# Kernel optimization log

Measured on AMD Instinct MI355X. Metric: run time of the kernel, lower is better.

Reference implementation:

```python
import jax, jax.numpy as jnp
import numpy as np
from jax import lax

STORAGE = 8
HIDDEN_HEAD = 32
N_BLOCKS = 16


def _conv(x, w, b, padding):
    # x: NCHW, w: OIHW
    y = lax.conv_general_dilated(
        x, w, window_strides=(1, 1), padding=padding,
        dimension_numbers=("NCHW", "OIHW", "NCHW"))
    return y + b[None, :, None, None]


def _min_pool3(x):
    # 3x3 sliding-window min, stride 1, same padding (pad value +inf so it
    return lax.reduce_window(x, float("inf"), lax.min,
                             (1, 1, 3, 3), (1, 1, 1, 1), "SAME")


def setup_inputs() -> dict:
    key = jax.random.key(0)
    ks = jax.random.split(key, 7)
    B, H, W = 8, 512, 512
    x = jax.random.normal(ks[0], (B, 1, H, W), dtype=jnp.float32)
    # initial 1x1 conv: 1 -> 8
    w0 = jax.random.normal(ks[1], (STORAGE, 1, 1, 1), dtype=jnp.float32) * 1.0
    b0 = jax.random.normal(ks[2], (STORAGE,), dtype=jnp.float32) * 0.1
    # head conv 3x3: 8 -> 32
    w1 = jax.random.normal(ks[3], (HIDDEN_HEAD, STORAGE, 3, 3), dtype=jnp.float32) * (1.0 / np.sqrt(STORAGE * 9))
    b1 = jax.random.normal(ks[4], (HIDDEN_HEAD,), dtype=jnp.float32) * 0.1
    # head conv 1x1: 32 -> 1
    w2 = jax.random.normal(ks[5], (1, HIDDEN_HEAD, 1, 1), dtype=jnp.float32) * (1.0 / np.sqrt(HIDDEN_HEAD))
    b2 = jax.random.normal(ks[6], (1,), dtype=jnp.float32) * 0.1
    return {"x": x, "w0": w0, "b0": b0, "w1": w1, "b1": b1, "w2": w2, "b2": b2}


def reference(x, w0, b0, w1, b1, w2, b2):
    h = _conv(x, w0, b0, "SAME")  # [B,8,H,W]
    for _ in range(N_BLOCKS):
        h = h + _min_pool3(h)
    h = _conv(h, w1, b1, "SAME")  # [B,32,H,W]
    h = jax.nn.relu(h)
    return _conv(h, w2, b2, "SAME")  # [B,1,H,W]
```

## Files before the change

### kernel.cpp

```cpp
#include <hip/hip_runtime.h>
#include <math.h>


#define N_PIX (512*512)
#define INF __builtin_inff()

typedef __attribute__((ext_vector_type(2))) float f2;

__device__ __forceinline__ float dpp_shr1(float v, float fill) {
    return __int_as_float(__builtin_amdgcn_update_dpp(
        __float_as_int(fill), __float_as_int(v), 0x138, 0xF, 0xF, false));
}
__device__ __forceinline__ float dpp_shl1(float v, float fill) {
    return __int_as_float(__builtin_amdgcn_update_dpp(
        __float_as_int(fill), __float_as_int(v), 0x130, 0xF, 0xF, false));
}

struct Row8 { float4 a, b; };

__device__ __forceinline__ Row8 row_update8(const Row8 up, const Row8 mid, const Row8 dn)
{
    float4 va, vb;
    va.x = fminf(fminf(up.a.x, mid.a.x), dn.a.x);
    va.y = fminf(fminf(up.a.y, mid.a.y), dn.a.y);
    va.z = fminf(fminf(up.a.z, mid.a.z), dn.a.z);
    va.w = fminf(fminf(up.a.w, mid.a.w), dn.a.w);
    vb.x = fminf(fminf(up.b.x, mid.b.x), dn.b.x);
    vb.y = fminf(fminf(up.b.y, mid.b.y), dn.b.y);
    vb.z = fminf(fminf(up.b.z, mid.b.z), dn.b.z);
    vb.w = fminf(fminf(up.b.w, mid.b.w), dn.b.w);
    float vmL = dpp_shr1(vb.w, INF);
    float vmR = dpp_shl1(va.x, INF);
    float tm1 = fminf(vmL, va.x);
    float t0 = fminf(va.x, va.y), t1 = fminf(va.y, va.z);
    float t2 = fminf(va.z, va.w), t3 = fminf(va.w, vb.x);
    float t4 = fminf(vb.x, vb.y), t5 = fminf(vb.y, vb.z);
    float t6 = fminf(vb.z, vb.w), t7 = fminf(vb.w, vmR);
    Row8 o;
    o.a.x = mid.a.x + fminf(tm1, t0);
    o.a.y = mid.a.y + fminf(t0, t1);
    o.a.z = mid.a.z + fminf(t1, t2);
    o.a.w = mid.a.w + fminf(t2, t3);
    o.b.x = mid.b.x + fminf(t3, t4);
    o.b.y = mid.b.y + fminf(t4, t5);
    o.b.z = mid.b.z + fminf(t5, t6);
    o.b.w = mid.b.w + fminf(t6, t7);
    return o;
}

__device__ __forceinline__ void halo_write(f2* hp, const Row8& v) {
    hp[0*64] = (f2){v.a.x, v.a.y};
    hp[1*64] = (f2){v.a.z, v.a.w};
    hp[2*64] = (f2){v.b.x, v.b.y};
    hp[3*64] = (f2){v.b.z, v.b.w};
}
__device__ __forceinline__ Row8 halo_read(const f2* hp) {
    f2 p0 = hp[0*64], p1 = hp[1*64], p2 = hp[2*64], p3 = hp[3*64];
    Row8 v;
    v.a = make_float4(p0.x, p0.y, p1.x, p1.y);
    v.b = make_float4(p2.x, p2.y, p3.x, p3.y);
    return v;
}

__global__ __launch_bounds__(256, 1) void erode16_kernel(
    const float* __restrict__ x, float* __restrict__ A,
    const float* __restrict__ w0, const float* __restrict__ b0,
    const float* __restrict__ w1, const float* __restrict__ b1,
    float* __restrict__ W)
{
    if (blockIdx.x == 0 && blockIdx.y == 0) {
        for (int t = threadIdx.x; t < 288; t += 256) {
            int oc = t / 9, k = t - oc*9;
            float wp = 0.f, wq = 0.f;
            for (int ic = 0; ic < 8; ++ic) {
                float a = w0[ic];
                float w = w1[oc*72 + ic*9 + k];
                if (a > 0.f) wp += w * a;
                else         wq += w * (-a);
            }
            W[(oc*9 + k)*2 + 0] = wp;
            W[(oc*9 + k)*2 + 1] = wq;
            if (k == 0) {
                float beta[9];
                for (int kk = 0; kk < 9; ++kk) {
                    float s = 0.f;
                    for (int ic = 0; ic < 8; ++ic) s += b0[ic] * w1[oc*72 + ic*9 + kk];
                    beta[kk] = 65536.0f * s;
                }
                for (int r = 0; r < 3; ++r) {
                    W[576 + oc*4 + r] = beta[r*3] + beta[r*3+1] + beta[r*3+2]
                                      + ((r == 1) ? b1[oc] : 0.f);
                    W[704 + oc*4 + r] = beta[r*3 + 0];
                    W[832 + oc*4 + r] = beta[r*3 + 2];
                }
            }
        }
    }

    __shared__ f2 halo[2][4][2][4][64];
    const int tid   = threadIdx.x;
    const int lane  = tid & 63;
    const int w     = tid >> 6;
    const int ty    = blockIdx.x;
    const int plane = blockIdx.y;
    const int colg  = lane * 8;
    const int row0g = ty*32 - 16 + w*16;

    const float* sp = x + (plane & 7)*N_PIX;
    const float sgn = (plane >= 8) ? -1.f : 1.f;

    Row8 h[16];
    #pragma unroll
    for (int r = 0; r < 16; ++r) {
        int gy = row0g + r;
        if ((unsigned)gy < 512u) {
            const float* rp = sp + gy*512 + colg;
            float4 a = *(const float4*)rp;
            float4 b = *(const float4*)(rp + 4);
            h[r].a = make_float4(a.x*sgn, a.y*sgn, a.z*sgn, a.w*sgn);
            h[r].b = make_float4(b.x*sgn, b.y*sgn, b.z*sgn, b.w*sgn);
        } else {
            h[r].a = make_float4(INF, INF, INF, INF);
            h[r].b = h[r].a;
        }
    }

    const Row8 inf8 = { make_float4(INF,INF,INF,INF), make_float4(INF,INF,INF,INF) };
    for (int s = 0; s < 16; ++s) {
        int par = s & 1;
        halo_write(&halo[par][w][0][0][lane], h[0]);
        halo_write(&halo[par][w][1][0][lane], h[15]);
        Row8 o1 = h[1];
        Row8 prev = h[0];
        #pragma unroll
        for (int r = 1; r <= 14; ++r) {
            Row8 tmp = h[r];
            h[r] = row_update8(prev, h[r], h[r+1]);
            prev = tmp;
        }
        __syncthreads();
        Row8 up = inf8, dn = inf8;
        if (w > 0) up = halo_read(&halo[par][w-1][1][0][lane]);
        if (w < 3) dn = halo_read(&halo[par][w+1][0][0][lane]);
        h[0]  = row_update8(up,   h[0],  o1);
        h[15] = row_update8(prev, h[15], dn);
    }

    if (w == 1 || w == 2) {
        float* dp = A + plane*N_PIX;
        #pragma unroll
        for (int r = 0; r < 16; ++r) {
            float* op = dp + (row0g + r)*512 + colg;
            *(float4*)op       = h[r].a;
            *(float4*)(op + 4) = h[r].b;
        }
    }
}

__global__ __launch_bounds__(256) void head_kernel(
    const float* __restrict__ A, const float* __restrict__ W,
    const float* __restrict__ w2, const float* __restrict__ b2,
    float* __restrict__ out)
{
    const int tid  = threadIdx.x;
    const int lane = tid & 63;
    const int w    = tid >> 6;
    const int img  = blockIdx.x >> 7;
    const int y    = (blockIdx.x & 127)*4 + w;
    const int x0   = lane*8;

    const float* P = A + img*N_PIX;
    const float* Q = A + (8 + img)*N_PIX;

    f2 pq[3][10];
    #pragma unroll
    for (int dy = 0; dy < 3; ++dy) {
        int gy = y + dy - 1;
        if ((unsigned)gy < 512u) {
            const float* rp = P + gy*512 + x0;
            const float* rq = Q + gy*512 + x0;
            float4 a = *(const float4*)rp;
            float4 b = *(const float4*)(rp + 4);
            float4 c = *(const float4*)rq;
            float4 d = *(const float4*)(rq + 4);
            pq[dy][1] = (f2){a.x, c.x}; pq[dy][2] = (f2){a.y, c.y};
            pq[dy][3] = (f2){a.z, c.z}; pq[dy][4] = (f2){a.w, c.w};
            pq[dy][5] = (f2){b.x, d.x}; pq[dy][6] = (f2){b.y, d.y};
            pq[dy][7] = (f2){b.z, d.z}; pq[dy][8] = (f2){b.w, d.w};
            pq[dy][0] = (f2){dpp_shr1(b.w, 0.f), dpp_shr1(d.w, 0.f)};
            pq[dy][9] = (f2){dpp_shl1(a.x, 0.f), dpp_shl1(c.x, 0.f)};
        } else {
            #pragma unroll
            for (int j = 0; j < 10; ++j) pq[dy][j] = (f2){0.f, 0.f};
        }
    }

    const float ry0 = (y >= 1)   ? 1.f : 0.f;
    const float ry2 = (y <= 510) ? 1.f : 0.f;
    const float mL  = (lane == 0)  ? -1.f : 0.f;
    const float mR  = (lane == 63) ? -1.f : 0.f;

    float o[8];
    #pragma unroll
    for (int j = 0; j < 8; ++j) o[j] = 0.f;

    const f2* Wv = (const f2*)W;
    #pragma unroll 2
    for (int oc = 0; oc < 32; ++oc) {
        f2 acc[8];
        {
            f2 wv0 = Wv[oc*9];
            #pragma unroll
            for (int j = 0; j < 8; ++j) acc[j] = wv0 * pq[0][j];
        }
        #pragma unroll
        for (int t = 1; t < 9; ++t) {
            const int ky = t / 3, kx = t - ky*3;
            f2 wv = Wv[oc*9 + t];
            #pragma unroll
            for (int j = 0; j < 8; ++j) acc[j] += wv * pq[ky][kx + j];
        }
        float base = W[576 + oc*4 + 1]
                   + ry0 * W[576 + oc*4 + 0]
                   + ry2 * W[576 + oc*4 + 2];
        float cl = W[704 + oc*4 + 1] + ry0 * W[704 + oc*4 + 0] + ry2 * W[704 + oc*4 + 2];
        float cr = W[832 + oc*4 + 1] + ry0 * W[832 + oc*4 + 0] + ry2 * W[832 + oc*4 + 2];
        float s[8];
        #pragma unroll
        for (int j = 0; j < 8; ++j) s[j] = acc[j].x + acc[j].y + base;
        s[0] = fmaf(cl, mL, s[0]);
        s[7] = fmaf(cr, mR, s[7]);
        float sc = w2[oc];
        #pragma unroll
        for (int j = 0; j < 8; ++j) o[j] += fmaxf(s[j], 0.f) * sc;
    }

    float bb = b2[0];
    float* op = out + img*N_PIX + y*512 + x0;
    *(float4*)(op)     = make_float4(o[0]+bb, o[1]+bb, o[2]+bb, o[3]+bb);
    *(float4*)(op + 4) = make_float4(o[4]+bb, o[5]+bb, o[6]+bb, o[7]+bb);
}

extern "C" void kernel_launch(void* const* d_in, const int* in_sizes, int n_in,
                              void* d_out, int out_size, void* d_ws, size_t ws_size,
                              hipStream_t stream) {
    const float* x  = (const float*)d_in[0];
    const float* w0 = (const float*)d_in[1];
    const float* b0 = (const float*)d_in[2];
    const float* w1 = (const float*)d_in[3];
    const float* b1 = (const float*)d_in[4];
    const float* w2 = (const float*)d_in[5];
    const float* b2 = (const float*)d_in[6];
    float* out = (float*)d_out;

    float* wsf = (float*)d_ws;
    float* A = wsf;
    float* W = wsf + 16*N_PIX;

    dim3 eg(16, 16);
    erode16_kernel<<<eg, 256, 0, stream>>>(x, A, w0, b0, w1, b1, W);

    head_kernel<<<1024, 256, 0, stream>>>(A, W, w2, b2, out);
}
```

Measured before the change: 130.8 us.

## Split erosion rows across 16 waves per block and precompute boundary bias tables

```diff
diff --git a/kernel.cpp b/kernel.cpp
--- a/kernel.cpp
+++ b/kernel.cpp
@@ -62,56 +62,65 @@
     return v;
 }
 
-__global__ __launch_bounds__(256, 1) void erode16_kernel(
+__global__ __launch_bounds__(1024, 4) void erode16_kernel(
     const float* __restrict__ x, float* __restrict__ A,
     const float* __restrict__ w0, const float* __restrict__ b0,
     const float* __restrict__ w1, const float* __restrict__ b1,
     float* __restrict__ W)
 {
-    if (blockIdx.x == 0 && blockIdx.y == 0) {
-        for (int t = threadIdx.x; t < 288; t += 256) {
-            int oc = t / 9, k = t - oc*9;
-            float wp = 0.f, wq = 0.f;
-            for (int ic = 0; ic < 8; ++ic) {
-                float a = w0[ic];
-                float w = w1[oc*72 + ic*9 + k];
-                if (a > 0.f) wp += w * a;
-                else         wq += w * (-a);
+    if (blockIdx.x == 0 && blockIdx.y == 0 && threadIdx.x < 288) {
+        int tid = threadIdx.x;
+        int oc = tid / 9, k = tid - oc*9;
+        float wp = 0.f, wq = 0.f;
+        for (int ic = 0; ic < 8; ++ic) {
+            float a = w0[ic];
+            float w = w1[oc*72 + ic*9 + k];
+            if (a > 0.f) wp += w * a;
+            else         wq += w * (-a);
+        }
+        W[(oc*9 + k)*2 + 0] = wp;
+        W[(oc*9 + k)*2 + 1] = wq;
+        if (k == 0) {
+            float beta[9];
+            for (int kk = 0; kk < 9; ++kk) {
+                float s = 0.f;
+                for (int ic = 0; ic < 8; ++ic) s += b0[ic] * w1[oc*72 + ic*9 + kk];
+                beta[kk] = 65536.0f * s;
             }
-            W[(oc*9 + k)*2 + 0] = wp;
-            W[(oc*9 + k)*2 + 1] = wq;
-            if (k == 0) {
-                float beta[9];
-                for (int kk = 0; kk < 9; ++kk) {
-                    float s = 0.f;
-                    for (int ic = 0; ic < 8; ++ic) s += b0[ic] * w1[oc*72 + ic*9 + kk];
-                    beta[kk] = 65536.0f * s;
-                }
-                for (int r = 0; r < 3; ++r) {
-                    W[576 + oc*4 + r] = beta[r*3] + beta[r*3+1] + beta[r*3+2]
-                                      + ((r == 1) ? b1[oc] : 0.f);
-                    W[704 + oc*4 + r] = beta[r*3 + 0];
-                    W[832 + oc*4 + r] = beta[r*3 + 2];
-                }
+            float R[3], L[3], Rr[3];
+            for (int r = 0; r < 3; ++r) {
+                R[r]  = beta[r*3] + beta[r*3+1] + beta[r*3+2];
+                L[r]  = beta[r*3 + 0];
+                Rr[r] = beta[r*3 + 2];
             }
-        }
-    }
-
-    __shared__ f2 halo[2][4][2][4][64];
+            float bb = b1[oc];
+            W[576 + 0*96 + oc]      = bb + R[1] + R[2];
+            W[576 + 0*96 + 32 + oc] = L[1] + L[2];
+            W[576 + 0*96 + 64 + oc] = Rr[1] + Rr[2];
+            W[576 + 1*96 + oc]      = bb + R[0] + R[1] + R[2];
+            W[576 + 1*96 + 32 + oc] = L[0] + L[1] + L[2];
+            W[576 + 1*96 + 64 + oc] = Rr[0] + Rr[1] + Rr[2];
+            W[576 + 2*96 + oc]      = bb + R[0] + R[1];
+            W[576 + 2*96 + 32 + oc] = L[0] + L[1];
+            W[576 + 2*96 + 64 + oc] = Rr[0] + Rr[1];
+        }
+    }
+
+    __shared__ f2 halo[2][16][2][4][64];
     const int tid   = threadIdx.x;
     const int lane  = tid & 63;
     const int w     = tid >> 6;
     const int ty    = blockIdx.x;
     const int plane = blockIdx.y;
     const int colg  = lane * 8;
-    const int row0g = ty*32 - 16 + w*16;
+    const int row0g = ty*32 - 16 + w*4;
 
     const float* sp = x + (plane & 7)*N_PIX;
     const float sgn = (plane >= 8) ? -1.f : 1.f;
 
-    Row8 h[16];
+    Row8 h[4];
     #pragma unroll
-    for (int r = 0; r < 16; ++r) {
+    for (int r = 0; r < 4; ++r) {
         int gy = row0g + r;
         if ((unsigned)gy < 512u) {
             const float* rp = sp + gy*512 + colg;
@@ -129,27 +138,27 @@
     for (int s = 0; s < 16; ++s) {
         int par = s & 1;
         halo_write(&halo[par][w][0][0][lane], h[0]);
-        halo_write(&halo[par][w][1][0][lane], h[15]);
+        halo_write(&halo[par][w][1][0][lane], h[3]);
         Row8 o1 = h[1];
         Row8 prev = h[0];
         #pragma unroll
-        for (int r = 1; r <= 14; ++r) {
+        for (int r = 1; r <= 2; ++r) {
             Row8 tmp = h[r];
             h[r] = row_update8(prev, h[r], h[r+1]);
             prev = tmp;
         }
         __syncthreads();
         Row8 up = inf8, dn = inf8;
-        if (w > 0) up = halo_read(&halo[par][w-1][1][0][lane]);
-        if (w < 3) dn = halo_read(&halo[par][w+1][0][0][lane]);
-        h[0]  = row_update8(up,   h[0],  o1);
-        h[15] = row_update8(prev, h[15], dn);
-    }
-
-    if (w == 1 || w == 2) {
+        if (w > 0)  up = halo_read(&halo[par][w-1][1][0][lane]);
+        if (w < 15) dn = halo_read(&halo[par][w+1][0][0][lane]);
+        h[0] = row_update8(up,   h[0], o1);
+        h[3] = row_update8(prev, h[3], dn);
+    }
+
+    if (w >= 4 && w <= 11) {
         float* dp = A + plane*N_PIX;
         #pragma unroll
-        for (int r = 0; r < 16; ++r) {
+        for (int r = 0; r < 4; ++r) {
             float* op = dp + (row0g + r)*512 + colg;
             *(float4*)op       = h[r].a;
             *(float4*)(op + 4) = h[r].b;
@@ -195,8 +204,8 @@
         }
     }
 
-    const float ry0 = (y >= 1)   ? 1.f : 0.f;
-    const float ry2 = (y <= 510) ? 1.f : 0.f;
+    const int wcase = (y == 0) ? 0 : ((y == 511) ? 2 : 1);
+    const float* WB = W + 576 + wcase*96;
     const float mL  = (lane == 0)  ? -1.f : 0.f;
     const float mR  = (lane == 63) ? -1.f : 0.f;
 
@@ -220,11 +229,9 @@
             #pragma unroll
             for (int j = 0; j < 8; ++j) acc[j] += wv * pq[ky][kx + j];
         }
-        float base = W[576 + oc*4 + 1]
-                   + ry0 * W[576 + oc*4 + 0]
-                   + ry2 * W[576 + oc*4 + 2];
-        float cl = W[704 + oc*4 + 1] + ry0 * W[704 + oc*4 + 0] + ry2 * W[704 + oc*4 + 2];
-        float cr = W[832 + oc*4 + 1] + ry0 * W[832 + oc*4 + 0] + ry2 * W[832 + oc*4 + 2];
+        float base = WB[oc];
+        float cl   = WB[32 + oc];
+        float cr   = WB[64 + oc];
         float s[8];
         #pragma unroll
         for (int j = 0; j < 8; ++j) s[j] = acc[j].x + acc[j].y + base;
@@ -258,7 +265,7 @@
     float* W = wsf + 16*N_PIX;
 
     dim3 eg(16, 16);
-    erode16_kernel<<<eg, 256, 0, stream>>>(x, A, w0, b0, w1, b1, W);
+    erode16_kernel<<<eg, 1024, 0, stream>>>(x, A, w0, b0, w1, b1, W);
 
     head_kernel<<<1024, 256, 0, stream>>>(A, W, w2, b2, out);
 }
```

Result: faster. 125.9 us (-3.7%).
